# Kernel tuning notes

Hardware: AMD Instinct MI355X
Metric: run time of the kernel (lower is better)

The kernel has to match this reference:

```python
import jax, jax.numpy as jnp
import numpy as np

N_NODES = 50000
N_EDGES = 800000


def setup_inputs() -> dict:
    key = jax.random.key(0)
    ks = jax.random.split(key, 8)
    N, E, F_IN, D1, D2, K = N_NODES, N_EDGES, 128, 256, 128, 32
    return {
        "features": jax.random.normal(ks[0], (N, F_IN), dtype=jnp.float32),
        "edges": jax.random.randint(ks[1], (2, E), 0, N, dtype=jnp.int64),
        "W1": jax.random.normal(ks[2], (F_IN, D1), dtype=jnp.float32) * (1.0 / np.sqrt(F_IN)),
        "b1": jax.random.normal(ks[3], (D1,), dtype=jnp.float32) * 0.01,
        "fc1_W": jax.random.normal(ks[4], (D1, D2), dtype=jnp.float32) * (1.0 / np.sqrt(D1)),
        "fc1_b": jax.random.normal(ks[5], (D2,), dtype=jnp.float32) * 0.01,
        "fc2_W": jax.random.normal(ks[6], (D2, K), dtype=jnp.float32) * (1.0 / np.sqrt(D2)),
        "fc2_b": jax.random.normal(ks[7], (K,), dtype=jnp.float32) * 0.01,
    }


def _gcn_conv(x, edges, W, b, num_nodes):
    # PyG GCNConv: x' = D^{-1/2} (A + I) D^{-1/2} (x W) + b, edge_weight = 1
    row, col = edges[0], edges[1]  # row = source j, col = target i
    loop = jnp.arange(num_nodes, dtype=row.dtype)
    r = jnp.concatenate([row, loop])
    c = jnp.concatenate([col, loop])
    w = jnp.ones(r.shape[0], dtype=x.dtype)
    deg = jax.ops.segment_sum(w, c, num_segments=num_nodes)
    dinv = jnp.where(deg > 0, jax.lax.rsqrt(jnp.maximum(deg, 1e-30)), 0.0)
    norm = dinv[r] * dinv[c]  # [E+N]
    xw = x @ W  # [N, D1]
    out = jax.ops.segment_sum(norm[:, None] * xw[r], c, num_segments=num_nodes)
    return out + b


def _forward(features, edges, W1, b1, fc1_W, fc1_b, fc2_W, fc2_b):
    N = features.shape[0]
    row, col = edges[0], edges[1]

    # GCN layer (only graph_convolution_1 is used in forward)
    H = _gcn_conv(features, edges, W1, b1, N)  # [N, D1]

    abstract = jnp.tanh(H @ fc1_W + fc1_b)  # [N, D2]
    S = jax.nn.softmax(abstract @ fc2_W + fc2_b, axis=1)  # [N, K] cluster assignment

    # Symmetric Laplacian L = I - D^{-1/2} A D^{-1/2}, edge_weight = 1
    ew = jnp.ones(row.shape[0], dtype=features.dtype)
    deg = jax.ops.segment_sum(ew, row, num_segments=N)
    dinv = jnp.where(deg > 0, jax.lax.rsqrt(jnp.maximum(deg, 1e-30)), 0.0)
    wl = -(dinv[row] * dinv[col])  # off-diagonal Laplacian weights
    # L @ S = I*S + scatter of off-diagonal contributions
    LS = S + jax.ops.segment_sum(wl[:, None] * S[col], row, num_segments=N)  # [N, K]

    new_adj = S.T @ LS  # [K, K]
    row_sums = jnp.sum(jnp.abs(new_adj), axis=1, keepdims=True)
    normalize_new_adj = new_adj / jnp.maximum(row_sums, 1e-12)  # F.normalize p=1 dim=1
    norm_diag = jnp.diagonal(normalize_new_adj)  # [K]
    eye = jnp.eye(norm_diag.shape[0], dtype=features.dtype)
    # torch MSELoss broadcasts [K] against [K,K] -> mean over K*K elements
    pos_penalty = jnp.mean((norm_diag - eye) ** 2)

    graph_embedding = S.T @ H  # [K, D1]
    graph_embedding = jnp.mean(graph_embedding, axis=0, keepdims=True)  # [1, D1]
    return graph_embedding, pos_penalty


def reference(features, edges, W1, b1, fc1_W, fc1_b, fc2_W, fc2_b):
    return _forward(features, edges, W1, b1, fc1_W, fc1_b, fc2_W, fc2_b)
```

## Files before the change

### kernel.cpp

```cpp
#include <hip/hip_runtime.h>
#include <math.h>

#define FIN 128
#define D1  256
#define D2  128
#define KCL 32
#define CAP 8192

typedef __attribute__((ext_vector_type(8))) short short8;
typedef __attribute__((ext_vector_type(4))) float floatx4;

__device__ __forceinline__ ushort f2bf(float f) {
    unsigned u = __float_as_uint(f);
    unsigned r = (u + 0x7fffu + ((u >> 16) & 1u)) >> 16;
    return (ushort)r;
}
__device__ __forceinline__ float bf2f(ushort h) {
    return __uint_as_float(((unsigned)h) << 16);
}

__global__ __launch_bounds__(256) void k_p1w(const int* __restrict__ edges, int E, int NBIN,
                                             int* __restrict__ gcnt, unsigned* __restrict__ binbuf,
                                             const float* __restrict__ W1, const float* __restrict__ fc1W,
                                             const float* __restrict__ b1, const float* __restrict__ fc1b,
                                             const float* __restrict__ fc2W,
                                             ushort* __restrict__ Wct, float* __restrict__ bc,
                                             ushort* __restrict__ W2t) {
    int dir = blockIdx.y;
    int t = threadIdx.x;
    __shared__ int h[256], base[256], cur[256];
    __shared__ float fcol[2][256];

    if (dir == 2) {
        if (blockIdx.x < 64) {
            int k = t & 127, hh = t >> 7;
            int n = blockIdx.x * 2 + hh;
            fcol[hh][k] = fc1W[k * 128 + n];
            fcol[hh][k + 128] = fc1W[(k + 128) * 128 + n];
            __syncthreads();
            float a = 0.f;
            for (int m = 0; m < 256; m++) a += W1[k * 256 + m] * fcol[hh][m];
            Wct[n * 128 + k] = f2bf(a);
            if (k == 0) {
                float bb = fc1b[n];
                for (int m = 0; m < 256; m++) bb += b1[m] * fcol[hh][m];
                bc[n] = bb;
            }
        } else if (blockIdx.x == 64) {
#pragma unroll
            for (int i = 0; i < 16; i++) {
                int idx = t + i * 256;
                int k = idx >> 5, n = idx & 31;
                float wv = fc2W[idx];
                ushort hi = f2bf(wv);
                ushort lo = f2bf(wv - bf2f(hi));
                W2t[n * 128 + k] = hi;
                W2t[KCL * D2 + n * 128 + k] = lo;
            }
        }
        return;
    }

    h[t] = 0;
    __syncthreads();
    int chunk = (E + gridDim.x - 1) / gridDim.x;
    int lo = blockIdx.x * chunk, hi = min(lo + chunk, E);
    const int* keys = dir ? edges : edges + E;
    for (int e = lo + t; e < hi; e += 256) atomicAdd(&h[keys[e] >> 8], 1);
    __syncthreads();
    if (t < NBIN) { base[t] = atomicAdd(&gcnt[dir * NBIN + t], h[t]); }
    cur[t] = 0;
    __syncthreads();
    unsigned* bb = binbuf + (size_t)dir * NBIN * CAP;
    for (int e = lo + t; e < hi; e += 256) {
        int r = edges[e], c = edges[E + e];
        int key = dir ? r : c;
        unsigned payload = dir ? ((unsigned)c | ((unsigned)(r & 255) << 16))
                               : ((unsigned)r | ((unsigned)(c & 255) << 16));
        int b = key >> 8;
        int pos = base[b] + atomicAdd(&cur[b], 1);
        if (pos < CAP) bb[(size_t)b * CAP + pos] = payload;
    }
}

__global__ __launch_bounds__(256) void k_p2(const unsigned* __restrict__ binbuf, const int* __restrict__ gcnt,
                                            int N, int E, int NBIN,
                                            int* __restrict__ col_ptr, int* __restrict__ row_ptr,
                                            ushort* __restrict__ col_idx, ushort* __restrict__ row_idx,
                                            float* __restrict__ dinv1, float* __restrict__ dinv2) {
    int d = blockIdx.y, b = blockIdx.x, t = threadIdx.x;
    __shared__ int sc[256], h[256], hx[256], cur[256];
    sc[t] = (t < NBIN) ? gcnt[d * NBIN + t] : 0;
    __syncthreads();
    for (int st = 1; st < 256; st <<= 1) {
        int u = (t >= st) ? sc[t - st] : 0;
        __syncthreads();
        sc[t] += u;
        __syncthreads();
    }
    int cnt_b = gcnt[d * NBIN + b];
    int binbase = sc[b] - cnt_b;
    h[t] = 0;
    __syncthreads();
    const unsigned* bb = binbuf + ((size_t)d * NBIN + b) * CAP;
    int m = min(cnt_b, CAP);
    for (int i = t; i < m; i += 256) atomicAdd(&h[bb[i] >> 16], 1);
    __syncthreads();
    int hv = h[t];
    hx[t] = hv;
    __syncthreads();
    for (int st = 1; st < 256; st <<= 1) {
        int u = (t >= st) ? hx[t - st] : 0;
        __syncthreads();
        hx[t] += u;
        __syncthreads();
    }
    int excl = hx[t] - hv;
    int node = b * 256 + t;
    if (node < N) {
        if (d == 0) {
            dinv1[node] = rsqrtf((float)hv + 1.0f);
            col_ptr[node] = binbase + excl;
            if (node == N - 1) col_ptr[N] = E;
        } else {
            dinv2[node] = hv ? rsqrtf((float)hv) : 0.0f;
            row_ptr[node] = binbase + excl;
            if (node == N - 1) row_ptr[N] = E;
        }
    }
    hx[t] = excl;
    cur[t] = 0;
    __syncthreads();
    ushort* oidx = d ? row_idx : col_idx;
    for (int i = t; i < m; i += 256) {
        unsigned p = bb[i];
        int nl = p >> 16;
        int rk = atomicAdd(&cur[nl], 1);
        oidx[binbase + hx[nl] + rk] = (ushort)(p & 0xffff);
    }
}

__global__ void k_v(const int* __restrict__ row_ptr, const ushort* __restrict__ row_idx,
                    const float* __restrict__ dinv1, float* __restrict__ v, int N) {
    int j = blockIdx.x * blockDim.x + threadIdx.x;
    if (j >= N) return;
    int lo = row_ptr[j], hi = row_ptr[j + 1];
    float s0 = dinv1[j], s1 = 0.f, s2 = 0.f, s3 = 0.f;
    int e = lo;
    for (; e + 4 <= hi; e += 4) {
        int i0 = row_idx[e], i1 = row_idx[e + 1], i2 = row_idx[e + 2], i3 = row_idx[e + 3];
        s0 += dinv1[i0]; s1 += dinv1[i1]; s2 += dinv1[i2]; s3 += dinv1[i3];
    }
    for (; e < hi; e++) s0 += dinv1[row_idx[e]];
    v[j] = dinv1[j] * ((s0 + s1) + (s2 + s3));
}

__global__ __launch_bounds__(256) void k_prep(const float* __restrict__ X, const float* __restrict__ dinv1,
                                              const float* __restrict__ vvec,
                                              unsigned* __restrict__ Xs2, float* __restrict__ xsum, int N) {
    int t = threadIdx.x;
    int cp = t & 63;
    int rg = t >> 6;
    float s0 = 0.f, s1 = 0.f;
    for (int j0 = blockIdx.x * 4; j0 < N; j0 += gridDim.x * 4) {
        int j = j0 + rg;
        if (j < N) {
            float2 x = ((const float2*)X)[(long)j * 64 + cp];
            float d = dinv1[j];
            Xs2[(long)j * 64 + cp] = (unsigned)f2bf(d * x.x) | ((unsigned)f2bf(d * x.y) << 16);
            float v = vvec[j];
            s0 += v * x.x;
            s1 += v * x.y;
        }
    }
    __shared__ float red[256][2];
    red[t][0] = s0; red[t][1] = s1;
    __syncthreads();
    if (rg == 0) {
        float r0 = red[cp][0] + red[64 + cp][0] + red[128 + cp][0] + red[192 + cp][0];
        float r1 = red[cp][1] + red[64 + cp][1] + red[128 + cp][1] + red[192 + cp][1];
        atomicAdd(&xsum[2 * cp], r0);
        atomicAdd(&xsum[2 * cp + 1], r1);
    }
}

__global__ __launch_bounds__(256) void k_aggX(const unsigned* __restrict__ Xs2,
                                              const int* __restrict__ col_ptr, const ushort* __restrict__ col_idx,
                                              const float* __restrict__ dinv1,
                                              unsigned* __restrict__ aggX2, int N) {
    int wv = threadIdx.x >> 6, l = threadIdx.x & 63;
    int i = blockIdx.x * 4 + wv;
    if (i >= N) return;
    int lo = col_ptr[i], hi = col_ptr[i + 1];
    unsigned p0 = Xs2[(long)i * 64 + l];
    float a0 = bf2f((ushort)(p0 & 0xffff));
    float a1 = bf2f((ushort)(p0 >> 16));
    float b0 = 0.f, b1v = 0.f, c0 = 0.f, c1 = 0.f, d0 = 0.f, d1 = 0.f;
    int e = lo;
    for (; e + 8 <= hi; e += 8) {
        int s0 = col_idx[e + 0], s1 = col_idx[e + 1], s2 = col_idx[e + 2], s3 = col_idx[e + 3];
        int s4 = col_idx[e + 4], s5 = col_idx[e + 5], s6 = col_idx[e + 6], s7 = col_idx[e + 7];
        unsigned q0 = Xs2[(long)s0 * 64 + l];
        unsigned q1 = Xs2[(long)s1 * 64 + l];
        unsigned q2 = Xs2[(long)s2 * 64 + l];
        unsigned q3 = Xs2[(long)s3 * 64 + l];
        unsigned q4 = Xs2[(long)s4 * 64 + l];
        unsigned q5 = Xs2[(long)s5 * 64 + l];
        unsigned q6 = Xs2[(long)s6 * 64 + l];
        unsigned q7 = Xs2[(long)s7 * 64 + l];
        a0 += bf2f((ushort)(q0 & 0xffff)); a1 += bf2f((ushort)(q0 >> 16));
        b0 += bf2f((ushort)(q1 & 0xffff)); b1v += bf2f((ushort)(q1 >> 16));
        c0 += bf2f((ushort)(q2 & 0xffff)); c1 += bf2f((ushort)(q2 >> 16));
        d0 += bf2f((ushort)(q3 & 0xffff)); d1 += bf2f((ushort)(q3 >> 16));
        a0 += bf2f((ushort)(q4 & 0xffff)); a1 += bf2f((ushort)(q4 >> 16));
        b0 += bf2f((ushort)(q5 & 0xffff)); b1v += bf2f((ushort)(q5 >> 16));
        c0 += bf2f((ushort)(q6 & 0xffff)); c1 += bf2f((ushort)(q6 >> 16));
        d0 += bf2f((ushort)(q7 & 0xffff)); d1 += bf2f((ushort)(q7 >> 16));
    }
    for (; e < hi; e++) {
        int s = col_idx[e];
        unsigned q = Xs2[(long)s * 64 + l];
        a0 += bf2f((ushort)(q & 0xffff));
        a1 += bf2f((ushort)(q >> 16));
    }
    a0 = (a0 + b0) + (c0 + d0);
    a1 = (a1 + b1v) + (c1 + d1);
    float d = dinv1[i];
    aggX2[(long)i * 64 + l] = (unsigned)f2bf(d * a0) | ((unsigned)f2bf(d * a1) << 16);
}

template <int KTOT, int NC>
__global__ __launch_bounds__(256) void k_gemm_fused(
    const ushort* __restrict__ A, const ushort* __restrict__ Bt,
    const float* __restrict__ bias,
    const ushort* __restrict__ W2t,
    const float* __restrict__ b2,
    const float* __restrict__ dinv2,
    float* __restrict__ Sm, ushort* __restrict__ z, int N)
{
    constexpr int NT = NC / 16;
    __shared__ union alignas(16) SMem {
        ushort Bs[NC * KTOT];
        struct { ushort ab[64][132]; ushort W2h[KCL * D2]; ushort W2l[KCL * D2]; } s2;
    } u;
    int t = threadIdx.x;
    constexpr int CPR = KTOT / 8;
    for (int idx = t; idx < NC * CPR; idx += 256) {
        int n = idx / CPR, c = idx % CPR;
        int cs = c ^ (n & 15);
        *(short8*)&u.Bs[n * KTOT + cs * 8] = *(const short8*)&Bt[(long)n * KTOT + c * 8];
    }
    __syncthreads();

    int wave = t >> 6, lane = t & 63;
    int quad = lane >> 4, l15 = lane & 15;
    int arow = blockIdx.x * 64 + wave * 16 + l15;
    long aoff_row = (long)min(arow, N - 1) * KTOT;

    floatx4 acc[NT];
#pragma unroll
    for (int tt = 0; tt < NT; tt++) acc[tt] = {0.f, 0.f, 0.f, 0.f};

    for (int k0 = 0; k0 < KTOT; k0 += 32) {
        short8 af = *(const short8*)&A[aoff_row + k0 + quad * 8];
#pragma unroll
        for (int tt = 0; tt < NT; tt++) {
            int n = tt * 16 + l15;
            int cix = ((k0 >> 3) + quad) ^ (n & 15);
            short8 bf = *(const short8*)&u.Bs[n * KTOT + cix * 8];
            acc[tt] = __builtin_amdgcn_mfma_f32_16x16x32_bf16(af, bf, acc[tt], 0, 0, 0);
        }
    }

    __syncthreads();
    int rloc = wave * 16 + quad * 4;
#pragma unroll
    for (int r = 0; r < 4; r++) {
#pragma unroll
        for (int tt = 0; tt < NT; tt++) {
            int c = tt * 16 + l15;
            u.s2.ab[rloc + r][c] = f2bf(tanhf(acc[tt][r] + bias[c]));
        }
    }
    for (int idx = t; idx < KCL * 16; idx += 256) {
        int n = idx >> 4, c = idx & 15;
        int cs = c ^ (n & 15);
        *(short8*)&u.s2.W2h[n * 128 + cs * 8] = *(const short8*)&W2t[n * 128 + c * 8];
        *(short8*)&u.s2.W2l[n * 128 + cs * 8] = *(const short8*)&W2t[KCL * D2 + n * 128 + c * 8];
    }
    __syncthreads();

    floatx4 p0 = {0.f, 0.f, 0.f, 0.f}, p1 = {0.f, 0.f, 0.f, 0.f};
    int abrow = wave * 16 + l15;
#pragma unroll
    for (int k0 = 0; k0 < KTOT; k0 += 32) {
        short8 af2 = *(const short8*)&u.s2.ab[abrow][k0 + quad * 8];
        int cix = ((k0 >> 3) + quad) ^ l15;
        short8 wh0 = *(const short8*)&u.s2.W2h[l15 * 128 + cix * 8];
        short8 wl0 = *(const short8*)&u.s2.W2l[l15 * 128 + cix * 8];
        short8 wh1 = *(const short8*)&u.s2.W2h[(16 + l15) * 128 + cix * 8];
        short8 wl1 = *(const short8*)&u.s2.W2l[(16 + l15) * 128 + cix * 8];
        p0 = __builtin_amdgcn_mfma_f32_16x16x32_bf16(af2, wh0, p0, 0, 0, 0);
        p0 = __builtin_amdgcn_mfma_f32_16x16x32_bf16(af2, wl0, p0, 0, 0, 0);
        p1 = __builtin_amdgcn_mfma_f32_16x16x32_bf16(af2, wh1, p1, 0, 0, 0);
        p1 = __builtin_amdgcn_mfma_f32_16x16x32_bf16(af2, wl1, p1, 0, 0, 0);
    }

    float b2a = b2[l15], b2b = b2[16 + l15];
#pragma unroll
    for (int r = 0; r < 4; r++) {
        int node = blockIdx.x * 64 + wave * 16 + quad * 4 + r;
        float v0 = p0[r] + b2a, v1 = p1[r] + b2b;
        float mx = fmaxf(v0, v1);
#pragma unroll
        for (int mask = 8; mask >= 1; mask >>= 1) mx = fmaxf(mx, __shfl_xor(mx, mask));
        float e0 = __expf(v0 - mx), e1 = __expf(v1 - mx);
        float s = e0 + e1;
#pragma unroll
        for (int mask = 8; mask >= 1; mask >>= 1) s += __shfl_xor(s, mask);
        float sv0 = e0 / s, sv1 = e1 / s;
        if (node < N) {
            Sm[(long)node * KCL + l15] = sv0;
            Sm[(long)node * KCL + 16 + l15] = sv1;
            float dz = dinv2[node];
            z[(long)node * KCL + l15] = f2bf(dz * sv0);
            z[(long)node * KCL + 16 + l15] = f2bf(dz * sv1);
        }
    }
}

__global__ __launch_bounds__(256) void k_LS(const float* __restrict__ Sm, const ushort* __restrict__ z,
                                            const int* __restrict__ row_ptr, const ushort* __restrict__ row_idx,
                                            const float* __restrict__ dinv2,
                                            float* __restrict__ LS, int N) {
    int g = threadIdx.x >> 5;
    int l = threadIdx.x & 31;
    int i = blockIdx.x * 8 + g;
    if (i >= N) return;
    int lo = row_ptr[i], hi = row_ptr[i + 1];
    float a0 = 0.f, a1 = 0.f, a2 = 0.f, a3 = 0.f;
    int e = lo;
    for (; e + 4 <= hi; e += 4) {
        int c0 = row_idx[e], c1 = row_idx[e + 1], c2 = row_idx[e + 2], c3 = row_idx[e + 3];
        a0 += bf2f(z[(long)c0 * KCL + l]);
        a1 += bf2f(z[(long)c1 * KCL + l]);
        a2 += bf2f(z[(long)c2 * KCL + l]);
        a3 += bf2f(z[(long)c3 * KCL + l]);
    }
    for (; e < hi; e++) a0 += bf2f(z[(long)row_idx[e] * KCL + l]);
    float acc = (a0 + a1) + (a2 + a3);
    LS[(long)i * KCL + l] = Sm[(long)i * KCL + l] - dinv2[i] * acc;
}

__global__ __launch_bounds__(256) void k_newadj_final(
    const float* __restrict__ S, const float* __restrict__ LS,
    float* __restrict__ newadj, const float* __restrict__ xsum,
    const float* __restrict__ W1, const float* __restrict__ b1,
    int* __restrict__ done, float* __restrict__ out, int N)
{
    __shared__ float Ss[8][32], Ls[8][32];
    __shared__ float srs[32], sdg[32], xs[FIN], nd[32];
    __shared__ int lastflag;
    int t = threadIdx.x;
    int l = t & 31, k0 = t >> 5;
    float acc[4] = {0.f, 0.f, 0.f, 0.f};
    for (int i0 = blockIdx.x * 8; i0 < N; i0 += gridDim.x * 8) {
        int m = min(8, N - i0);
        if (t < m * 32) {
            Ss[t >> 5][t & 31] = S[(long)i0 * KCL + t];
            Ls[t >> 5][t & 31] = LS[(long)i0 * KCL + t];
        }
        __syncthreads();
        for (int n = 0; n < m; n++) {
            float lv = Ls[n][l];
#pragma unroll
            for (int j = 0; j < 4; j++) acc[j] += Ss[n][k0 + 8 * j] * lv;
        }
        __syncthreads();
    }
#pragma unroll
    for (int j = 0; j < 4; j++) atomicAdd(&newadj[(k0 + 8 * j) * 32 + l], acc[j]);
    __threadfence();
    if (t == 0) lastflag = (atomicAdd(done, 1) == (int)gridDim.x - 1);
    __syncthreads();
    if (!lastflag) return;

    if (t < 32) srs[t] = 0.f;
    if (t < FIN) xs[t] = xsum[t];
    __syncthreads();
    float vv[4];
    float rsum = 0.f;
    int row = t >> 3, colb = (t & 7) * 4;
#pragma unroll
    for (int q = 0; q < 4; q++) {
        vv[q] = atomicAdd(&newadj[t * 4 + q], 0.0f);
        rsum += fabsf(vv[q]);
    }
    atomicAdd(&srs[row], rsum);
#pragma unroll
    for (int q = 0; q < 4; q++) if (colb + q == row) sdg[row] = vv[q];
    __syncthreads();
    if (t < 32) nd[t] = sdg[t] / fmaxf(srs[t], 1e-12f);
    __syncthreads();
    float acc2 = (float)N * b1[t];
    for (int k = 0; k < FIN; k++) acc2 += xs[k] * W1[k * D1 + t];
    out[t] = acc2 * (1.0f / 32.0f);
    if (t == 0) {
        float p = 0.f;
        for (int j = 0; j < 32; j++) {
            float d = nd[j];
            p += 31.0f * d * d + (d - 1.0f) * (d - 1.0f);
        }
        out[256] = p / 1024.0f;
    }
}

extern "C" void kernel_launch(void* const* d_in, const int* in_sizes, int n_in,
                              void* d_out, int out_size, void* d_ws, size_t ws_size,
                              hipStream_t stream) {
    const float* X     = (const float*)d_in[0];
    const int*   edges = (const int*)d_in[1];
    const float* W1    = (const float*)d_in[2];
    const float* b1    = (const float*)d_in[3];
    const float* fc1_W = (const float*)d_in[4];
    const float* fc1_b = (const float*)d_in[5];
    const float* fc2_W = (const float*)d_in[6];
    const float* fc2_b = (const float*)d_in[7];
    float* out = (float*)d_out;

    int N = in_sizes[0] / FIN;
    int E = in_sizes[1] / 2;
    int NBIN = (N + 255) >> 8;

    char* w = (char*)d_ws;
    auto carve = [&](size_t bytes) -> void* {
        void* p = (void*)w;
        w += (bytes + 255) & ~(size_t)255;
        return p;
    };
    ushort* Xs      = (ushort*)carve((size_t)N * FIN * 2);
    ushort* aggX    = (ushort*)carve((size_t)N * FIN * 2);
    unsigned* binbuf= (unsigned*)carve((size_t)2 * NBIN * CAP * 4);
    float* Sm       = (float*)carve((size_t)N * KCL * 4);
    ushort* zm      = (ushort*)carve((size_t)N * KCL * 2);
    float* dinv1    = (float*)carve((size_t)N * 4);
    float* dinv2    = (float*)carve((size_t)N * 4);
    float* vvec     = (float*)carve((size_t)N * 4);
    int* col_ptr    = (int*)carve((size_t)(N + 1) * 4);
    int* row_ptr    = (int*)carve((size_t)(N + 1) * 4);
    ushort* col_idx = (ushort*)carve((size_t)E * 2);
    ushort* row_idx = (ushort*)carve((size_t)E * 2);
    ushort* Wct     = (ushort*)carve((size_t)FIN * D2 * 2);
    float* bc       = (float*)carve((size_t)D2 * 4);
    ushort* W2t     = (ushort*)carve((size_t)2 * KCL * D2 * 2);
    float* accum    = (float*)carve((size_t)(1024 + 128 + 512) * 4);
    float* newadj   = accum;
    float* xsum     = accum + 1024;
    int*   gcnt     = (int*)(accum + 1024 + 128);
    int*   done     = gcnt + 500;
    float* LSm      = (float*)binbuf;

    hipMemsetAsync(accum, 0, (size_t)(1024 + 128 + 512) * 4, stream);

    k_p1w<<<dim3(256, 3), 256, 0, stream>>>(edges, E, NBIN, gcnt, binbuf,
                                            W1, fc1_W, b1, fc1_b, fc2_W, Wct, bc, W2t);
    k_p2<<<dim3(NBIN, 2), 256, 0, stream>>>(binbuf, gcnt, N, E, NBIN,
                                            col_ptr, row_ptr, col_idx, row_idx, dinv1, dinv2);
    k_v<<<(N + 255) / 256, 256, 0, stream>>>(row_ptr, row_idx, dinv1, vvec, N);
    k_prep<<<256, 256, 0, stream>>>(X, dinv1, vvec, (unsigned*)Xs, xsum, N);
    k_aggX<<<(N + 3) / 4, 256, 0, stream>>>((const unsigned*)Xs, col_ptr, col_idx, dinv1,
                                            (unsigned*)aggX, N);
    k_gemm_fused<FIN, D2><<<(N + 63) / 64, 256, 0, stream>>>(aggX, Wct, bc, W2t,
                                                             fc2_b, dinv2, Sm, zm, N);
    k_LS<<<(N + 7) / 8, 256, 0, stream>>>(Sm, zm, row_ptr, row_idx, dinv2, LSm, N);
    k_newadj_final<<<256, 256, 0, stream>>>(Sm, LSm, newadj, xsum, W1, b1, done, out, N);
}
```

Baseline: 263.4 us.

## Compute S^T L S via edge-wise MFMA and drop row-CSR build

Rewrites new_adj = S^T S - sum over edges z_r z_c^T, where z = dinv2*S. Each edge contributes an outer product, so the whole term is accumulated with split-bf16 (hi/lo) MFMA over node blocks and edge blocks. This removes the second CSR build (row direction), the k_v and k_LS kernels and the fp32 S and LS buffers. Degree and v are now computed with global atomics over edges, and a sentinel zero row handles padding. The cost is 4 MFMAs per 16 edges, with gathered uncoalesced loads of Zh/Zl per edge and atomic contention on vtmp and deg2.

```diff
diff --git a/kernel.cpp b/kernel.cpp
--- a/kernel.cpp
+++ b/kernel.cpp
@@ -9,6 +9,7 @@
 
 typedef __attribute__((ext_vector_type(8))) short short8;
 typedef __attribute__((ext_vector_type(4))) float floatx4;
+typedef __attribute__((ext_vector_type(16))) float floatx16;
 
 __device__ __forceinline__ ushort f2bf(float f) {
     unsigned u = __float_as_uint(f);
@@ -31,7 +32,7 @@
     __shared__ int h[256], base[256], cur[256];
     __shared__ float fcol[2][256];
 
-    if (dir == 2) {
+    if (dir == 1) {
         if (blockIdx.x < 64) {
             int k = t & 127, hh = t >> 7;
             int n = blockIdx.x * 2 + hh;
@@ -65,32 +66,28 @@
     __syncthreads();
     int chunk = (E + gridDim.x - 1) / gridDim.x;
     int lo = blockIdx.x * chunk, hi = min(lo + chunk, E);
-    const int* keys = dir ? edges : edges + E;
+    const int* keys = edges + E;
     for (int e = lo + t; e < hi; e += 256) atomicAdd(&h[keys[e] >> 8], 1);
     __syncthreads();
-    if (t < NBIN) { base[t] = atomicAdd(&gcnt[dir * NBIN + t], h[t]); }
+    if (t < NBIN) { base[t] = atomicAdd(&gcnt[t], h[t]); }
     cur[t] = 0;
     __syncthreads();
-    unsigned* bb = binbuf + (size_t)dir * NBIN * CAP;
     for (int e = lo + t; e < hi; e += 256) {
         int r = edges[e], c = edges[E + e];
-        int key = dir ? r : c;
-        unsigned payload = dir ? ((unsigned)c | ((unsigned)(r & 255) << 16))
-                               : ((unsigned)r | ((unsigned)(c & 255) << 16));
-        int b = key >> 8;
+        unsigned payload = (unsigned)r | ((unsigned)(c & 255) << 16);
+        int b = c >> 8;
         int pos = base[b] + atomicAdd(&cur[b], 1);
-        if (pos < CAP) bb[(size_t)b * CAP + pos] = payload;
+        if (pos < CAP) binbuf[(size_t)b * CAP + pos] = payload;
     }
 }
 
 __global__ __launch_bounds__(256) void k_p2(const unsigned* __restrict__ binbuf, const int* __restrict__ gcnt,
                                             int N, int E, int NBIN,
-                                            int* __restrict__ col_ptr, int* __restrict__ row_ptr,
-                                            ushort* __restrict__ col_idx, ushort* __restrict__ row_idx,
-                                            float* __restrict__ dinv1, float* __restrict__ dinv2) {
-    int d = blockIdx.y, b = blockIdx.x, t = threadIdx.x;
+                                            int* __restrict__ col_ptr, ushort* __restrict__ col_idx,
+                                            float* __restrict__ dinv1) {
+    int b = blockIdx.x, t = threadIdx.x;
     __shared__ int sc[256], h[256], hx[256], cur[256];
-    sc[t] = (t < NBIN) ? gcnt[d * NBIN + t] : 0;
+    sc[t] = (t < NBIN) ? gcnt[t] : 0;
     __syncthreads();
     for (int st = 1; st < 256; st <<= 1) {
         int u = (t >= st) ? sc[t - st] : 0;
@@ -98,11 +95,11 @@
         sc[t] += u;
         __syncthreads();
     }
-    int cnt_b = gcnt[d * NBIN + b];
+    int cnt_b = gcnt[b];
     int binbase = sc[b] - cnt_b;
     h[t] = 0;
     __syncthreads();
-    const unsigned* bb = binbuf + ((size_t)d * NBIN + b) * CAP;
+    const unsigned* bb = binbuf + (size_t)b * CAP;
     int m = min(cnt_b, CAP);
     for (int i = t; i < m; i += 256) atomicAdd(&h[bb[i] >> 16], 1);
     __syncthreads();
@@ -118,47 +115,41 @@
     int excl = hx[t] - hv;
     int node = b * 256 + t;
     if (node < N) {
-        if (d == 0) {
-            dinv1[node] = rsqrtf((float)hv + 1.0f);
-            col_ptr[node] = binbase + excl;
-            if (node == N - 1) col_ptr[N] = E;
-        } else {
-            dinv2[node] = hv ? rsqrtf((float)hv) : 0.0f;
-            row_ptr[node] = binbase + excl;
-            if (node == N - 1) row_ptr[N] = E;
-        }
+        dinv1[node] = rsqrtf((float)hv + 1.0f);
+        col_ptr[node] = binbase + excl;
+        if (node == N - 1) col_ptr[N] = E;
     }
     hx[t] = excl;
     cur[t] = 0;
     __syncthreads();
-    ushort* oidx = d ? row_idx : col_idx;
     for (int i = t; i < m; i += 256) {
         unsigned p = bb[i];
         int nl = p >> 16;
         int rk = atomicAdd(&cur[nl], 1);
-        oidx[binbase + hx[nl] + rk] = (ushort)(p & 0xffff);
-    }
-}
-
-__global__ void k_v(const int* __restrict__ row_ptr, const ushort* __restrict__ row_idx,
-                    const float* __restrict__ dinv1, float* __restrict__ v, int N) {
-    int j = blockIdx.x * blockDim.x + threadIdx.x;
-    if (j >= N) return;
-    int lo = row_ptr[j], hi = row_ptr[j + 1];
-    float s0 = dinv1[j], s1 = 0.f, s2 = 0.f, s3 = 0.f;
-    int e = lo;
-    for (; e + 4 <= hi; e += 4) {
-        int i0 = row_idx[e], i1 = row_idx[e + 1], i2 = row_idx[e + 2], i3 = row_idx[e + 3];
-        s0 += dinv1[i0]; s1 += dinv1[i1]; s2 += dinv1[i2]; s3 += dinv1[i3];
-    }
-    for (; e < hi; e++) s0 += dinv1[row_idx[e]];
-    v[j] = dinv1[j] * ((s0 + s1) + (s2 + s3));
+        col_idx[binbase + hx[nl] + rk] = (ushort)(p & 0xffff);
+    }
+}
+
+__global__ __launch_bounds__(256) void k_vd(const int* __restrict__ edges, int E,
+                                            const float* __restrict__ dinv1,
+                                            float* __restrict__ vtmp, int* __restrict__ deg2) {
+    int e = blockIdx.x * 256 + threadIdx.x;
+    if (e >= E) return;
+    int r = edges[e], c = edges[E + e];
+    atomicAdd(&vtmp[r], dinv1[c]);
+    atomicAdd(&deg2[r], 1);
 }
 
 __global__ __launch_bounds__(256) void k_prep(const float* __restrict__ X, const float* __restrict__ dinv1,
-                                              const float* __restrict__ vvec,
-                                              unsigned* __restrict__ Xs2, float* __restrict__ xsum, int N) {
+                                              const float* __restrict__ vtmp, const int* __restrict__ deg2,
+                                              float* __restrict__ dinv2,
+                                              unsigned* __restrict__ Xs2, float* __restrict__ xsum,
+                                              ushort* __restrict__ Sh, ushort* __restrict__ Sl,
+                                              ushort* __restrict__ Zh, ushort* __restrict__ Zl, int N) {
     int t = threadIdx.x;
+    if (blockIdx.x == 0 && t < 32) {
+        Sh[N * 32 + t] = 0; Sl[N * 32 + t] = 0; Zh[N * 32 + t] = 0; Zl[N * 32 + t] = 0;
+    }
     int cp = t & 63;
     int rg = t >> 6;
     float s0 = 0.f, s1 = 0.f;
@@ -168,9 +159,13 @@
             float2 x = ((const float2*)X)[(long)j * 64 + cp];
             float d = dinv1[j];
             Xs2[(long)j * 64 + cp] = (unsigned)f2bf(d * x.x) | ((unsigned)f2bf(d * x.y) << 16);
-            float v = vvec[j];
-            s0 += v * x.x;
-            s1 += v * x.y;
+            float vj = d * (d + vtmp[j]);
+            s0 += vj * x.x;
+            s1 += vj * x.y;
+            if (cp == 0) {
+                int dg = deg2[j];
+                dinv2[j] = dg ? rsqrtf((float)dg) : 0.0f;
+            }
         }
     }
     __shared__ float red[256][2];
@@ -236,7 +231,8 @@
     const ushort* __restrict__ W2t,
     const float* __restrict__ b2,
     const float* __restrict__ dinv2,
-    float* __restrict__ Sm, ushort* __restrict__ z, int N)
+    ushort* __restrict__ Sh, ushort* __restrict__ Sl,
+    ushort* __restrict__ Zh, ushort* __restrict__ Zl, int N)
 {
     constexpr int NT = NC / 16;
     __shared__ union alignas(16) SMem {
@@ -320,91 +316,112 @@
         for (int mask = 8; mask >= 1; mask >>= 1) s += __shfl_xor(s, mask);
         float sv0 = e0 / s, sv1 = e1 / s;
         if (node < N) {
-            Sm[(long)node * KCL + l15] = sv0;
-            Sm[(long)node * KCL + 16 + l15] = sv1;
             float dz = dinv2[node];
-            z[(long)node * KCL + l15] = f2bf(dz * sv0);
-            z[(long)node * KCL + 16 + l15] = f2bf(dz * sv1);
-        }
-    }
-}
-
-__global__ __launch_bounds__(256) void k_LS(const float* __restrict__ Sm, const ushort* __restrict__ z,
-                                            const int* __restrict__ row_ptr, const ushort* __restrict__ row_idx,
-                                            const float* __restrict__ dinv2,
-                                            float* __restrict__ LS, int N) {
-    int g = threadIdx.x >> 5;
-    int l = threadIdx.x & 31;
-    int i = blockIdx.x * 8 + g;
-    if (i >= N) return;
-    int lo = row_ptr[i], hi = row_ptr[i + 1];
-    float a0 = 0.f, a1 = 0.f, a2 = 0.f, a3 = 0.f;
-    int e = lo;
-    for (; e + 4 <= hi; e += 4) {
-        int c0 = row_idx[e], c1 = row_idx[e + 1], c2 = row_idx[e + 2], c3 = row_idx[e + 3];
-        a0 += bf2f(z[(long)c0 * KCL + l]);
-        a1 += bf2f(z[(long)c1 * KCL + l]);
-        a2 += bf2f(z[(long)c2 * KCL + l]);
-        a3 += bf2f(z[(long)c3 * KCL + l]);
-    }
-    for (; e < hi; e++) a0 += bf2f(z[(long)row_idx[e] * KCL + l]);
-    float acc = (a0 + a1) + (a2 + a3);
-    LS[(long)i * KCL + l] = Sm[(long)i * KCL + l] - dinv2[i] * acc;
-}
-
-__global__ __launch_bounds__(256) void k_newadj_final(
-    const float* __restrict__ S, const float* __restrict__ LS,
+            ushort h0 = f2bf(sv0);
+            ushort h1 = f2bf(sv1);
+            Sh[node * 32 + l15] = h0;      Sl[node * 32 + l15] = f2bf(sv0 - bf2f(h0));
+            Sh[node * 32 + 16 + l15] = h1; Sl[node * 32 + 16 + l15] = f2bf(sv1 - bf2f(h1));
+            float z0 = dz * sv0, z1 = dz * sv1;
+            ushort g0 = f2bf(z0);
+            ushort g1 = f2bf(z1);
+            Zh[node * 32 + l15] = g0;      Zl[node * 32 + l15] = f2bf(z0 - bf2f(g0));
+            Zh[node * 32 + 16 + l15] = g1; Zl[node * 32 + 16 + l15] = f2bf(z1 - bf2f(g1));
+        }
+    }
+}
+
+__global__ __launch_bounds__(1024) void k_adj_final(
+    const int* __restrict__ edges, int E, int N,
+    const ushort* __restrict__ Sh, const ushort* __restrict__ Sl,
+    const ushort* __restrict__ Zh, const ushort* __restrict__ Zl,
     float* __restrict__ newadj, const float* __restrict__ xsum,
     const float* __restrict__ W1, const float* __restrict__ b1,
-    int* __restrict__ done, float* __restrict__ out, int N)
+    int* __restrict__ done, float* __restrict__ out)
 {
-    __shared__ float Ss[8][32], Ls[8][32];
+    int t = threadIdx.x;
+    int wv = t >> 6, l = t & 63;
+    int half = l >> 5, a = l & 31;
+    int NBn = (N + 15) >> 4, NBe = (E + 15) >> 4;
+    int NBT = NBn + NBe;
+    floatx16 acc;
+#pragma unroll
+    for (int r = 0; r < 16; r++) acc[r] = 0.f;
+
+    for (int g = blockIdx.x * 16 + wv; g < NBT; g += gridDim.x * 16) {
+        short8 Ah, Al, Bh, Bl;
+        if (g < NBn) {
+            int base = g * 16 + half * 8;
+#pragma unroll
+            for (int jj = 0; jj < 8; jj++) {
+                int node = base + jj;
+                int idx = (node < N) ? node : N;
+                Ah[jj] = (short)Sh[idx * 32 + a];
+                Al[jj] = (short)Sl[idx * 32 + a];
+            }
+            Bh = Ah; Bl = Al;
+        } else {
+            int e0 = (g - NBn) * 16 + half * 8;
+#pragma unroll
+            for (int jj = 0; jj < 8; jj++) {
+                int e = e0 + jj;
+                int sA = (e < E) ? edges[e] : N;
+                int sB = (e < E) ? edges[E + e] : N;
+                Ah[jj] = (short)(Zh[sA * 32 + a] ^ 0x8000u);
+                Al[jj] = (short)(Zl[sA * 32 + a] ^ 0x8000u);
+                Bh[jj] = (short)Zh[sB * 32 + a];
+                Bl[jj] = (short)Zl[sB * 32 + a];
+            }
+        }
+        acc = __builtin_amdgcn_mfma_f32_32x32x16_bf16(Ah, Bh, acc, 0, 0, 0);
+        acc = __builtin_amdgcn_mfma_f32_32x32x16_bf16(Ah, Bl, acc, 0, 0, 0);
+        acc = __builtin_amdgcn_mfma_f32_32x32x16_bf16(Al, Bh, acc, 0, 0, 0);
+        acc = __builtin_amdgcn_mfma_f32_32x32x16_bf16(Al, Bl, acc, 0, 0, 0);
+    }
+
+    __shared__ float red[4][1024];
+    for (int i = t; i < 4096; i += 1024) ((float*)red)[i] = 0.f;
+    __syncthreads();
+#pragma unroll
+    for (int r = 0; r < 16; r++) {
+        int row = (r & 3) + 8 * (r >> 2) + 4 * half;
+        atomicAdd(&red[wv & 3][row * 32 + a], acc[r]);
+    }
+    __syncthreads();
+    if (t < 1024) {
+        float s = (red[0][t] + red[1][t]) + (red[2][t] + red[3][t]);
+        atomicAdd(&newadj[t], s);
+    }
+    __threadfence();
+    __shared__ int lastflag;
+    if (t == 0) lastflag = (atomicAdd(done, 1) == (int)gridDim.x - 1);
+    __syncthreads();
+    if (!lastflag) return;
+
     __shared__ float srs[32], sdg[32], xs[FIN], nd[32];
-    __shared__ int lastflag;
-    int t = threadIdx.x;
-    int l = t & 31, k0 = t >> 5;
-    float acc[4] = {0.f, 0.f, 0.f, 0.f};
-    for (int i0 = blockIdx.x * 8; i0 < N; i0 += gridDim.x * 8) {
-        int m = min(8, N - i0);
-        if (t < m * 32) {
-            Ss[t >> 5][t & 31] = S[(long)i0 * KCL + t];
-            Ls[t >> 5][t & 31] = LS[(long)i0 * KCL + t];
-        }
-        __syncthreads();
-        for (int n = 0; n < m; n++) {
-            float lv = Ls[n][l];
-#pragma unroll
-            for (int j = 0; j < 4; j++) acc[j] += Ss[n][k0 + 8 * j] * lv;
-        }
-        __syncthreads();
-    }
-#pragma unroll
-    for (int j = 0; j < 4; j++) atomicAdd(&newadj[(k0 + 8 * j) * 32 + l], acc[j]);
-    __threadfence();
-    if (t == 0) lastflag = (atomicAdd(done, 1) == (int)gridDim.x - 1);
-    __syncthreads();
-    if (!lastflag) return;
-
     if (t < 32) srs[t] = 0.f;
     if (t < FIN) xs[t] = xsum[t];
     __syncthreads();
-    float vv[4];
-    float rsum = 0.f;
-    int row = t >> 3, colb = (t & 7) * 4;
-#pragma unroll
-    for (int q = 0; q < 4; q++) {
-        vv[q] = atomicAdd(&newadj[t * 4 + q], 0.0f);
-        rsum += fabsf(vv[q]);
-    }
-    atomicAdd(&srs[row], rsum);
-#pragma unroll
-    for (int q = 0; q < 4; q++) if (colb + q == row) sdg[row] = vv[q];
+    if (t < 256) {
+        float vv[4];
+        float rsum = 0.f;
+        int row = t >> 3, colb = (t & 7) * 4;
+#pragma unroll
+        for (int q = 0; q < 4; q++) {
+            vv[q] = atomicAdd(&newadj[t * 4 + q], 0.0f);
+            rsum += fabsf(vv[q]);
+        }
+        atomicAdd(&srs[row], rsum);
+#pragma unroll
+        for (int q = 0; q < 4; q++) if (colb + q == row) sdg[row] = vv[q];
+    }
     __syncthreads();
     if (t < 32) nd[t] = sdg[t] / fmaxf(srs[t], 1e-12f);
     __syncthreads();
-    float acc2 = (float)N * b1[t];
-    for (int k = 0; k < FIN; k++) acc2 += xs[k] * W1[k * D1 + t];
-    out[t] = acc2 * (1.0f / 32.0f);
+    if (t < 256) {
+        float acc2 = (float)N * b1[t];
+        for (int k = 0; k < FIN; k++) acc2 += xs[k] * W1[k * D1 + t];
+        out[t] = acc2 * (1.0f / 32.0f);
+    }
     if (t == 0) {
         float p = 0.f;
         for (int j = 0; j < 32; j++) {
@@ -440,38 +457,39 @@
     };
     ushort* Xs      = (ushort*)carve((size_t)N * FIN * 2);
     ushort* aggX    = (ushort*)carve((size_t)N * FIN * 2);
-    unsigned* binbuf= (unsigned*)carve((size_t)2 * NBIN * CAP * 4);
-    float* Sm       = (float*)carve((size_t)N * KCL * 4);
-    ushort* zm      = (ushort*)carve((size_t)N * KCL * 2);
+    unsigned* binbuf= (unsigned*)carve((size_t)NBIN * CAP * 4);
+    ushort* Sh      = (ushort*)carve((size_t)(N + 1) * KCL * 2);
+    ushort* Sl      = (ushort*)carve((size_t)(N + 1) * KCL * 2);
+    ushort* Zh      = (ushort*)carve((size_t)(N + 1) * KCL * 2);
+    ushort* Zl      = (ushort*)carve((size_t)(N + 1) * KCL * 2);
     float* dinv1    = (float*)carve((size_t)N * 4);
     float* dinv2    = (float*)carve((size_t)N * 4);
-    float* vvec     = (float*)carve((size_t)N * 4);
     int* col_ptr    = (int*)carve((size_t)(N + 1) * 4);
-    int* row_ptr    = (int*)carve((size_t)(N + 1) * 4);
     ushort* col_idx = (ushort*)carve((size_t)E * 2);
-    ushort* row_idx = (ushort*)carve((size_t)E * 2);
     ushort* Wct     = (ushort*)carve((size_t)FIN * D2 * 2);
     float* bc       = (float*)carve((size_t)D2 * 4);
     ushort* W2t     = (ushort*)carve((size_t)2 * KCL * D2 * 2);
     float* accum    = (float*)carve((size_t)(1024 + 128 + 512) * 4);
+    int*   deg2     = (int*)carve((size_t)N * 4);
+    float* vtmp     = (float*)carve((size_t)N * 4);
     float* newadj   = accum;
     float* xsum     = accum + 1024;
     int*   gcnt     = (int*)(accum + 1024 + 128);
     int*   done     = gcnt + 500;
-    float* LSm      = (float*)binbuf;
-
-    hipMemsetAsync(accum, 0, (size_t)(1024 + 128 + 512) * 4, stream);
-
-    k_p1w<<<dim3(256, 3), 256, 0, stream>>>(edges, E, NBIN, gcnt, binbuf,
+
+    size_t nal = ((size_t)N * 4 + 255) & ~(size_t)255;
+    hipMemsetAsync(accum, 0, (size_t)(1024 + 128 + 512) * 4 + 2 * nal, stream);
+
+    k_p1w<<<dim3(256, 2), 256, 0, stream>>>(edges, E, NBIN, gcnt, binbuf,
                                             W1, fc1_W, b1, fc1_b, fc2_W, Wct, bc, W2t);
-    k_p2<<<dim3(NBIN, 2), 256, 0, stream>>>(binbuf, gcnt, N, E, NBIN,
-                                            col_ptr, row_ptr, col_idx, row_idx, dinv1, dinv2);
-    k_v<<<(N + 255) / 256, 256, 0, stream>>>(row_ptr, row_idx, dinv1, vvec, N);
-    k_prep<<<256, 256, 0, stream>>>(X, dinv1, vvec, (unsigned*)Xs, xsum, N);
+    k_p2<<<NBIN, 256, 0, stream>>>(binbuf, gcnt, N, E, NBIN, col_ptr, col_idx, dinv1);
+    k_vd<<<(E + 255) / 256, 256, 0, stream>>>(edges, E, dinv1, vtmp, deg2);
+    k_prep<<<256, 256, 0, stream>>>(X, dinv1, vtmp, deg2, dinv2, (unsigned*)Xs, xsum,
+                                    Sh, Sl, Zh, Zl, N);
     k_aggX<<<(N + 3) / 4, 256, 0, stream>>>((const unsigned*)Xs, col_ptr, col_idx, dinv1,
                                             (unsigned*)aggX, N);
     k_gemm_fused<FIN, D2><<<(N + 63) / 64, 256, 0, stream>>>(aggX, Wct, bc, W2t,
-                                                             fc2_b, dinv2, Sm, zm, N);
-    k_LS<<<(N + 7) / 8, 256, 0, stream>>>(Sm, zm, row_ptr, row_idx, dinv2, LSm, N);
-    k_newadj_final<<<256, 256, 0, stream>>>(Sm, LSm, newadj, xsum, W1, b1, done, out, N);
-}
+                                                             fc2_b, dinv2, Sh, Sl, Zh, Zl, N);
+    k_adj_final<<<256, 1024, 0, stream>>>(edges, E, N, Sh, Sl, Zh, Zl,
+                                          newadj, xsum, W1, b1, done, out);
+}
```

Result: slower. 415.6 us (+57.8%).
